# Optimization experiments

Measured on AMD Instinct MI355X. Metric: run time of the kernel, lower is better.

The kernel has to match this reference:

```python
import jax, jax.numpy as jnp
import numpy as np

N_NODES = 100000
N_EDGES = 1600000
IN_DIM = 256
OUT_DIM = 128


def setup_inputs() -> dict:
    key = jax.random.key(0)
    ks = jax.random.split(key, 8)
    x = jax.random.normal(ks[0], (N_NODES, IN_DIM), dtype=jnp.float32)
    # glorot-ish init scaling
    W = jax.random.normal(ks[1], (IN_DIM, OUT_DIM), dtype=jnp.float32) * (6.0 / (IN_DIM + OUT_DIM)) ** 0.5
    fsW = jax.random.normal(ks[2], (IN_DIM, OUT_DIM), dtype=jnp.float32) * (6.0 / (IN_DIM + OUT_DIM)) ** 0.5
    f_weights = jax.random.normal(ks[3], (2 * OUT_DIM, 1), dtype=jnp.float32) * (6.0 / (2 * OUT_DIM + 1)) ** 0.5
    f_bias = jnp.zeros((1,), dtype=jnp.float32)
    # degrees in [1, 64], strictly positive so pow(deg, -p) is finite
    dia_adj = jax.random.uniform(ks[4], (N_NODES,), dtype=jnp.float32) * 63.0 + 1.0
    row = jax.random.randint(ks[5], (N_EDGES,), 0, N_NODES, dtype=jnp.int32)
    col = jax.random.randint(ks[6], (N_EDGES,), 0, N_NODES, dtype=jnp.int32)
    return {"x": x, "W": W, "fsW": fsW, "f_weights": f_weights,
            "f_bias": f_bias, "dia_adj": dia_adj, "row": row, "col": col}


def reference(x, W, fsW, f_weights, f_bias, dia_adj, row, col):
    # pre_sup = x @ weights_, fpre_sup = x @ fs_weights  (dropout=0, dense inputs)
    pre_sup = x @ W                 # [N, out]
    fpre_sup = x @ fsW              # [N, out]
    d = W.shape[1]
    # concat([vi, vj]) @ f_weights == vi @ f_weights[:d] + vj @ f_weights[d:]
    wi, wj = f_weights[:d], f_weights[d:]
    score = jax.nn.sigmoid(fpre_sup[row] @ wi + fpre_sup[col] @ wj + f_bias)  # [E, 1]
    # degree-power normalization: (deg_i * deg_j) ** (-sigmoid_score)
    deg_vivj = (dia_adj[row] * dia_adj[col])[:, None]                         # [E, 1]
    vals = jnp.power(deg_vivj, -score)[:, 0]                                  # [E]
    # sparse matmul: out[r] += vals_e * pre_sup[c] for each edge e=(r,c)
    msg = vals[:, None] * pre_sup[col]                                        # [E, out]
    out = jax.ops.segment_sum(msg, row, num_segments=x.shape[0])              # [N, out]
    return jax.nn.relu(out)
```

## Files before the change

kernel.cpp:

```cpp
#include <hip/hip_runtime.h>

#define N_NODES 100000
#define N_EDGES 1600000
#define IN_DIM 256
#define OUT_DIM 128
#define BROWS 100
#define NBK 1000
#define PBLK 128
#define EPB 12500

typedef __attribute__((ext_vector_type(4))) float f32x4;
typedef __attribute__((ext_vector_type(8))) short s16x8;

__device__ inline unsigned short f2bf(float f) {
    union { float f; unsigned int u; } a; a.f = f;
    unsigned int r = a.u + 0x7fffu + ((a.u >> 16) & 1u);
    return (unsigned short)(r >> 16);
}
__device__ inline float bf2f(unsigned short h) {
    union { unsigned int u; float f; } a; a.u = ((unsigned int)h) << 16;
    return a.f;
}

__global__ __launch_bounds__(256) void kprep(
        const float* __restrict__ fsW, const float* __restrict__ fw,
        const float* __restrict__ W, const int* __restrict__ row,
        float* __restrict__ u, float* __restrict__ v,
        unsigned short* __restrict__ wt, int* __restrict__ hist_t) {
    __shared__ int h[NBK];
    __shared__ float wi[128], wj[128];
    const int t = threadIdx.x, blk = blockIdx.x;
    if (blk < PBLK) {
        wt[blk * 256 + t] = f2bf(W[(size_t)t * 128 + blk]);
        for (int b = t; b < NBK; b += 256) h[b] = 0;
        __syncthreads();
        const int e0 = blk * EPB;
        for (int i = t; i < EPB; i += 256)
            atomicAdd(&h[row[e0 + i] / BROWS], 1);
        __syncthreads();
        for (int b = t; b < NBK; b += 256)
            hist_t[b * PBLK + blk] = h[b];
    } else {
        if (t < 128) wi[t] = fw[t]; else wj[t - 128] = fw[t];
        __syncthreads();
        const float* rowp = fsW + (size_t)t * OUT_DIM;
        float su = 0.f, sv = 0.f;
        for (int d = 0; d < 128; d += 4) {
            float4 a = *(const float4*)(rowp + d);
            su += a.x * wi[d] + a.y * wi[d + 1] + a.z * wi[d + 2] + a.w * wi[d + 3];
            sv += a.x * wj[d] + a.y * wj[d + 1] + a.z * wj[d + 2] + a.w * wj[d + 3];
        }
        u[t] = su; v[t] = sv;
    }
}

__global__ __launch_bounds__(256) void gemm_mfma(
        const float* __restrict__ x, const unsigned short* __restrict__ wt,
        const float* __restrict__ u, const float* __restrict__ v,
        unsigned short* __restrict__ psb, float* __restrict__ si, float* __restrict__ sj) {
    __shared__ unsigned short xa[64 * 136];

    const int t = threadIdx.x;
    const int wave = t >> 6, lane = t & 63;
    const int l15 = lane & 15, lhi = lane >> 4;
    const int row = t >> 2, quad = t & 3;
    const int brow = blockIdx.x * 64;
    const int gnode = brow + row;
    const bool fullblk = (brow + 64 <= N_NODES);
    const bool valid = gnode < N_NODES;

    f32x4 acc[4][2];
#pragma unroll
    for (int mi = 0; mi < 4; ++mi)
#pragma unroll
        for (int ni = 0; ni < 2; ++ni) acc[mi][ni] = (f32x4){0.f, 0.f, 0.f, 0.f};
    float su = 0.f, sv = 0.f;

#pragma unroll
    for (int ph = 0; ph < 2; ++ph) {
        const float* xp = x + (size_t)gnode * IN_DIM + ph * 128 + quad * 32;
        const float* up = u + ph * 128 + quad * 32;
        const float* vp = v + ph * 128 + quad * 32;
        if (fullblk) {
#pragma unroll
            for (int cc = 0; cc < 4; ++cc) {
                float4 a0 = ((const float4*)xp)[cc * 2];
                float4 a1 = ((const float4*)xp)[cc * 2 + 1];
                float4 u0 = ((const float4*)up)[cc * 2], u1 = ((const float4*)up)[cc * 2 + 1];
                float4 v0 = ((const float4*)vp)[cc * 2], v1 = ((const float4*)vp)[cc * 2 + 1];
                su = fmaf(a0.x, u0.x, su); su = fmaf(a0.y, u0.y, su);
                su = fmaf(a0.z, u0.z, su); su = fmaf(a0.w, u0.w, su);
                su = fmaf(a1.x, u1.x, su); su = fmaf(a1.y, u1.y, su);
                su = fmaf(a1.z, u1.z, su); su = fmaf(a1.w, u1.w, su);
                sv = fmaf(a0.x, v0.x, sv); sv = fmaf(a0.y, v0.y, sv);
                sv = fmaf(a0.z, v0.z, sv); sv = fmaf(a0.w, v0.w, sv);
                sv = fmaf(a1.x, v1.x, sv); sv = fmaf(a1.y, v1.y, sv);
                sv = fmaf(a1.z, v1.z, sv); sv = fmaf(a1.w, v1.w, sv);
                union { unsigned short h[8]; uint4 q; } pk;
                pk.h[0] = f2bf(a0.x); pk.h[1] = f2bf(a0.y); pk.h[2] = f2bf(a0.z); pk.h[3] = f2bf(a0.w);
                pk.h[4] = f2bf(a1.x); pk.h[5] = f2bf(a1.y); pk.h[6] = f2bf(a1.z); pk.h[7] = f2bf(a1.w);
                *(uint4*)&xa[row * 136 + quad * 32 + cc * 8] = pk.q;
            }
        } else {
#pragma unroll
            for (int cc = 0; cc < 4; ++cc) {
                float4 a0 = make_float4(0.f, 0.f, 0.f, 0.f), a1 = a0;
                if (valid) {
                    a0 = ((const float4*)xp)[cc * 2];
                    a1 = ((const float4*)xp)[cc * 2 + 1];
                    float4 u0 = ((const float4*)up)[cc * 2], u1 = ((const float4*)up)[cc * 2 + 1];
                    float4 v0 = ((const float4*)vp)[cc * 2], v1 = ((const float4*)vp)[cc * 2 + 1];
                    su = fmaf(a0.x, u0.x, su); su = fmaf(a0.y, u0.y, su);
                    su = fmaf(a0.z, u0.z, su); su = fmaf(a0.w, u0.w, su);
                    su = fmaf(a1.x, u1.x, su); su = fmaf(a1.y, u1.y, su);
                    su = fmaf(a1.z, u1.z, su); su = fmaf(a1.w, u1.w, su);
                    sv = fmaf(a0.x, v0.x, sv); sv = fmaf(a0.y, v0.y, sv);
                    sv = fmaf(a0.z, v0.z, sv); sv = fmaf(a0.w, v0.w, sv);
                    sv = fmaf(a1.x, v1.x, sv); sv = fmaf(a1.y, v1.y, sv);
                    sv = fmaf(a1.z, v1.z, sv); sv = fmaf(a1.w, v1.w, sv);
                }
                union { unsigned short h[8]; uint4 q; } pk;
                pk.h[0] = f2bf(a0.x); pk.h[1] = f2bf(a0.y); pk.h[2] = f2bf(a0.z); pk.h[3] = f2bf(a0.w);
                pk.h[4] = f2bf(a1.x); pk.h[5] = f2bf(a1.y); pk.h[6] = f2bf(a1.z); pk.h[7] = f2bf(a1.w);
                *(uint4*)&xa[row * 136 + quad * 32 + cc * 8] = pk.q;
            }
        }
        __syncthreads();

        {
            const unsigned short* wb0 = wt + (size_t)(wave * 32 + l15) * IN_DIM + ph * 128 + lhi * 8;
            s16x8 bfr[4][2];
#pragma unroll
            for (int ks = 0; ks < 4; ++ks) {
                bfr[ks][0] = *(const s16x8*)(wb0 + ks * 32);
                bfr[ks][1] = *(const s16x8*)(wb0 + (size_t)16 * IN_DIM + ks * 32);
            }
#pragma unroll
            for (int ks = 0; ks < 4; ++ks) {
                const int k0 = ks * 32 + lhi * 8;
                s16x8 afr[4];
#pragma unroll
                for (int mi = 0; mi < 4; ++mi)
                    afr[mi] = *(const s16x8*)&xa[(mi * 16 + l15) * 136 + k0];
#pragma unroll
                for (int mi = 0; mi < 4; ++mi)
#pragma unroll
                    for (int ni = 0; ni < 2; ++ni)
                        acc[mi][ni] = __builtin_amdgcn_mfma_f32_16x16x32_bf16(
                            afr[mi], bfr[ks][ni], acc[mi][ni], 0, 0, 0);
            }
        }
        __syncthreads();
    }

    su += __shfl_xor(su, 1); su += __shfl_xor(su, 2);
    sv += __shfl_xor(sv, 1); sv += __shfl_xor(sv, 2);
    if (quad == 0 && valid) { si[gnode] = su; sj[gnode] = sv; }

    unsigned short* cl = xa;
#pragma unroll
    for (int mi = 0; mi < 4; ++mi)
#pragma unroll
        for (int ni = 0; ni < 2; ++ni) {
            const int colb = wave * 32 + ni * 16 + l15;
#pragma unroll
            for (int j = 0; j < 4; ++j)
                cl[(mi * 16 + lhi * 4 + j) * 128 + colb] = f2bf(acc[mi][ni][j]);
        }
    __syncthreads();
    {
        const int rl = t >> 2;
        const int cb = (t & 3) * 32;
        if (brow + rl < N_NODES) {
            const uint4* src = (const uint4*)&cl[rl * 128 + cb];
            uint4* dst = (uint4*)&psb[(size_t)(brow + rl) * OUT_DIM + cb];
            dst[0] = src[0]; dst[1] = src[1]; dst[2] = src[2]; dst[3] = src[3];
        }
    }
}

__global__ __launch_bounds__(1024) void kbscan(const int* __restrict__ hist_t,
                                               int* __restrict__ bpre) {
    __shared__ int s[1024];
    const int t = threadIdx.x;
    int v = 0;
    if (t < NBK) {
        const int* hp = hist_t + t * PBLK;
        for (int k = 0; k < PBLK; ++k) v += hp[k];
    }
    s[t] = v;
    __syncthreads();
    for (int off = 1; off < 1024; off <<= 1) {
        int nv = (t >= off) ? s[t - off] : 0;
        __syncthreads();
        s[t] += nv;
        __syncthreads();
    }
    if (t < NBK) bpre[t] = s[t] - v;
    if (t == 1023) bpre[NBK] = s[1023];
}

__global__ __launch_bounds__(128) void koff(const int* __restrict__ hist_t,
                                            const int* __restrict__ bpre,
                                            int* __restrict__ off) {
    const int b = blockIdx.x, t = threadIdx.x;
    const int lane = t & 63, w = t >> 6;
    int v = hist_t[b * PBLK + t];
    int s = v;
#pragma unroll
    for (int o = 1; o < 64; o <<= 1) { int tt = __shfl_up(s, o); if (lane >= o) s += tt; }
    __shared__ int ws2[2];
    if (lane == 63) ws2[w] = s;
    __syncthreads();
    int base = (w == 1) ? ws2[0] : 0;
    off[b * PBLK + t] = bpre[b] + base + (s - v);
}

__global__ __launch_bounds__(256) void kpart1(const int* __restrict__ row,
                                              const int* __restrict__ col,
                                              const int* __restrict__ off,
                                              unsigned int* __restrict__ part) {
    __shared__ int cur[NBK];
    const int t = threadIdx.x, blk = blockIdx.x;
    for (int b = t; b < NBK; b += 256) cur[b] = off[b * PBLK + blk];
    __syncthreads();
    const int e0 = blk * EPB;
    for (int i = t; i < EPB; i += 256) {
        int r = row[e0 + i], c = col[e0 + i];
        int b = r / BROWS;
        int rl = r - b * BROWS;
        int pos = atomicAdd(&cur[b], 1);
        part[pos] = ((unsigned)rl << 17) | (unsigned)c;
    }
}

__global__ __launch_bounds__(256) void kpart2(const unsigned int* __restrict__ part,
                                              const int* __restrict__ bpre,
                                              const float* __restrict__ si,
                                              const float* __restrict__ sj,
                                              const float* __restrict__ dia,
                                              const float* __restrict__ fb,
                                              int2* __restrict__ epack,
                                              int* __restrict__ offs,
                                              int* __restrict__ deg) {
    __shared__ int cnt[BROWS];
    __shared__ int cur[BROWS];
    __shared__ float sil[BROWS], dial[BROWS];
    __shared__ int wtot[4];
    const int b = blockIdx.x, t = threadIdx.x;
    const int rbase = b * BROWS;
    if (t < BROWS) {
        cnt[t] = 0;
        sil[t] = si[rbase + t];
        dial[t] = dia[rbase + t];
    }
    __syncthreads();
    const int bstart = bpre[b], bend = bpre[b + 1];
    for (int e = bstart + t; e < bend; e += 256)
        atomicAdd(&cnt[part[e] >> 17], 1);
    __syncthreads();
    {
        int vv = (t < BROWS) ? cnt[t] : 0;
        int lane = t & 63, w = t >> 6;
        int s = vv;
#pragma unroll
        for (int o = 1; o < 64; o <<= 1) { int tt = __shfl_up(s, o); if (lane >= o) s += tt; }
        if (lane == 63) wtot[w] = s;
        __syncthreads();
        int base = 0;
        for (int k = 0; k < w; ++k) base += wtot[k];
        int excl = base + s - vv;
        if (t < BROWS) {
            cur[t] = bstart + excl;
            offs[rbase + t] = bstart + excl;
            deg[rbase + t] = vv;
        }
    }
    __syncthreads();
    const float fbv = fb[0];
    for (int e = bstart + t; e < bend; e += 256) {
        unsigned pk = part[e];
        int rl = (int)(pk >> 17);
        int c = (int)(pk & 0x1FFFFu);
        float tval = sil[rl] + sj[c] + fbv;
        float sg = 1.f / (1.f + expf(-tval));
        float l2 = log2f(dial[rl] * dia[c]);
        float val = exp2f(-sg * l2);
        int pos = atomicAdd(&cur[rl], 1);
        epack[pos] = make_int2(c, __float_as_int(val));
    }
}

__global__ __launch_bounds__(256) void kgather(
        const int* __restrict__ offs, const int* __restrict__ deg,
        const int2* __restrict__ epack,
        const unsigned short* __restrict__ psb, float* __restrict__ out) {
    int lane = threadIdx.x & 31;
    int node = blockIdx.x * 8 + (threadIdx.x >> 5);
    if (node >= N_NODES) return;
    int start = offs[node], d = deg[node];
    const int2* ep = epack + start;
    float a0 = 0.f, a1 = 0.f, a2 = 0.f, a3 = 0.f;
    int k = 0;
    for (; k + 4 <= d; k += 4) {
        int2 e0 = ep[k], e1 = ep[k + 1], e2 = ep[k + 2], e3 = ep[k + 3];
        ushort4 p0 = *(const ushort4*)&psb[(size_t)e0.x * OUT_DIM + lane * 4];
        ushort4 p1 = *(const ushort4*)&psb[(size_t)e1.x * OUT_DIM + lane * 4];
        ushort4 p2 = *(const ushort4*)&psb[(size_t)e2.x * OUT_DIM + lane * 4];
        ushort4 p3 = *(const ushort4*)&psb[(size_t)e3.x * OUT_DIM + lane * 4];
        float v0 = __int_as_float(e0.y), v1 = __int_as_float(e1.y);
        float v2 = __int_as_float(e2.y), v3 = __int_as_float(e3.y);
        a0 = fmaf(v0, bf2f(p0.x), a0); a1 = fmaf(v0, bf2f(p0.y), a1);
        a2 = fmaf(v0, bf2f(p0.z), a2); a3 = fmaf(v0, bf2f(p0.w), a3);
        a0 = fmaf(v1, bf2f(p1.x), a0); a1 = fmaf(v1, bf2f(p1.y), a1);
        a2 = fmaf(v1, bf2f(p1.z), a2); a3 = fmaf(v1, bf2f(p1.w), a3);
        a0 = fmaf(v2, bf2f(p2.x), a0); a1 = fmaf(v2, bf2f(p2.y), a1);
        a2 = fmaf(v2, bf2f(p2.z), a2); a3 = fmaf(v2, bf2f(p2.w), a3);
        a0 = fmaf(v3, bf2f(p3.x), a0); a1 = fmaf(v3, bf2f(p3.y), a1);
        a2 = fmaf(v3, bf2f(p3.z), a2); a3 = fmaf(v3, bf2f(p3.w), a3);
    }
    for (; k < d; ++k) {
        int2 e0 = ep[k];
        float v0 = __int_as_float(e0.y);
        ushort4 p0 = *(const ushort4*)&psb[(size_t)e0.x * OUT_DIM + lane * 4];
        a0 = fmaf(v0, bf2f(p0.x), a0);
        a1 = fmaf(v0, bf2f(p0.y), a1);
        a2 = fmaf(v0, bf2f(p0.z), a2);
        a3 = fmaf(v0, bf2f(p0.w), a3);
    }
    float4 o;
    o.x = fmaxf(a0, 0.f); o.y = fmaxf(a1, 0.f);
    o.z = fmaxf(a2, 0.f); o.w = fmaxf(a3, 0.f);
    *(float4*)&out[(size_t)node * OUT_DIM + lane * 4] = o;
}

extern "C" void kernel_launch(void* const* d_in, const int* in_sizes, int n_in,
                              void* d_out, int out_size, void* d_ws, size_t ws_size,
                              hipStream_t stream) {
    const float* x   = (const float*)d_in[0];
    const float* W   = (const float*)d_in[1];
    const float* fsW = (const float*)d_in[2];
    const float* fw  = (const float*)d_in[3];
    const float* fb  = (const float*)d_in[4];
    const float* dia = (const float*)d_in[5];
    const int*   row = (const int*)d_in[6];
    const int*   col = (const int*)d_in[7];
    float* out = (float*)d_out;

    char* p = (char*)d_ws;
    auto alloc = [&](size_t bytes) -> char* {
        char* r = p; p += (bytes + 255) & ~(size_t)255; return r;
    };
    float* u      = (float*)alloc(256 * 4);
    float* v      = (float*)alloc(256 * 4);
    unsigned short* wtb = (unsigned short*)alloc((size_t)128 * 256 * 2);
    float* si     = (float*)alloc((size_t)N_NODES * 4);
    float* sj     = (float*)alloc((size_t)N_NODES * 4);
    int*   deg    = (int*)alloc((size_t)N_NODES * 4);
    int*   offs   = (int*)alloc((size_t)N_NODES * 4);
    unsigned short* psb = (unsigned short*)alloc((size_t)N_NODES * OUT_DIM * 2);
    int*   hist_t = (int*)alloc((size_t)NBK * PBLK * 4);
    int*   bpre   = (int*)alloc((size_t)(NBK + 1) * 4);
    int*   off    = (int*)alloc((size_t)NBK * PBLK * 4);
    unsigned int* part = (unsigned int*)alloc((size_t)N_EDGES * 4);
    int2*  epack  = (int2*)alloc((size_t)N_EDGES * 8);

    kprep<<<PBLK + 1, 256, 0, stream>>>(fsW, fw, W, row, u, v, wtb, hist_t);
    gemm_mfma<<<(N_NODES + 63) / 64, 256, 0, stream>>>(x, wtb, u, v, psb, si, sj);
    kbscan<<<1, 1024, 0, stream>>>(hist_t, bpre);
    koff<<<NBK, PBLK, 0, stream>>>(hist_t, bpre, off);
    kpart1<<<PBLK, 256, 0, stream>>>(row, col, off, part);
    kpart2<<<NBK, 256, 0, stream>>>(part, bpre, si, sj, dia, fb, epack, offs, deg);
    kgather<<<N_NODES / 8, 256, 0, stream>>>(offs, deg, epack, psb, out);
}
```

Before: 207.2 us.

## Split fp32-to-bf16 conversion from GEMM and load bf16 tiles via global_load_lds

Splits the fused convert+GEMM kernel in two. The first kernel converts x to a padded bf16 buffer and computes the score dot products. The second loads whole 64x256 bf16 tiles straight into LDS with global_load_lds, using an XOR swizzle against bank conflicts, and runs the MFMA loop without a mid-loop barrier. It also vectorizes the histogram-scan sum and unrolls the gather loop to 8 edges. The cost is an extra round trip of the bf16 x buffer through global memory (about 51 MB written and read) plus one more launch. The padded rows of that buffer are never written, so the GEMM reads uninitialised memory for those tail rows.

```diff
diff --git a/kernel.cpp b/kernel.cpp
--- a/kernel.cpp
+++ b/kernel.cpp
@@ -1,6 +1,7 @@
 #include <hip/hip_runtime.h>
 
 #define N_NODES 100000
+#define N_PAD 100032
 #define N_EDGES 1600000
 #define IN_DIM 256
 #define OUT_DIM 128
@@ -20,6 +21,11 @@
 __device__ inline float bf2f(unsigned short h) {
     union { unsigned int u; float f; } a; a.u = ((unsigned int)h) << 16;
     return a.f;
+}
+__device__ inline void gload16(const void* g, void* l) {
+    __builtin_amdgcn_global_load_lds(
+        (const __attribute__((address_space(1))) void*)g,
+        (__attribute__((address_space(3))) void*)l, 16, 0, 0);
 }
 
 __global__ __launch_bounds__(256) void kprep(
@@ -54,108 +60,101 @@
     }
 }
 
-__global__ __launch_bounds__(256) void gemm_mfma(
-        const float* __restrict__ x, const unsigned short* __restrict__ wt,
-        const float* __restrict__ u, const float* __restrict__ v,
-        unsigned short* __restrict__ psb, float* __restrict__ si, float* __restrict__ sj) {
-    __shared__ unsigned short xa[64 * 136];
+__global__ __launch_bounds__(256) void kconv(
+        const float* __restrict__ x, const float* __restrict__ u,
+        const float* __restrict__ v, unsigned short* __restrict__ xb,
+        float* __restrict__ si, float* __restrict__ sj) {
+    const int t = threadIdx.x;
+    const int row = t >> 2, quad = t & 3;
+    const int gnode = blockIdx.x * 64 + row;
+    if (gnode >= N_NODES) return;
+    const float* xp = x + (size_t)gnode * IN_DIM + quad * 64;
+    const float* up = u + quad * 64;
+    const float* vp = v + quad * 64;
+    unsigned short* op = xb + (size_t)gnode * IN_DIM + quad * 64;
+    float su = 0.f, sv = 0.f;
+#pragma unroll
+    for (int c = 0; c < 8; ++c) {
+        float4 a0 = ((const float4*)xp)[c * 2];
+        float4 a1 = ((const float4*)xp)[c * 2 + 1];
+        float4 u0 = ((const float4*)up)[c * 2], u1 = ((const float4*)up)[c * 2 + 1];
+        float4 v0 = ((const float4*)vp)[c * 2], v1 = ((const float4*)vp)[c * 2 + 1];
+        su = fmaf(a0.x, u0.x, su); su = fmaf(a0.y, u0.y, su);
+        su = fmaf(a0.z, u0.z, su); su = fmaf(a0.w, u0.w, su);
+        su = fmaf(a1.x, u1.x, su); su = fmaf(a1.y, u1.y, su);
+        su = fmaf(a1.z, u1.z, su); su = fmaf(a1.w, u1.w, su);
+        sv = fmaf(a0.x, v0.x, sv); sv = fmaf(a0.y, v0.y, sv);
+        sv = fmaf(a0.z, v0.z, sv); sv = fmaf(a0.w, v0.w, sv);
+        sv = fmaf(a1.x, v1.x, sv); sv = fmaf(a1.y, v1.y, sv);
+        sv = fmaf(a1.z, v1.z, sv); sv = fmaf(a1.w, v1.w, sv);
+        union { unsigned short h[8]; uint4 q; } pk;
+        pk.h[0] = f2bf(a0.x); pk.h[1] = f2bf(a0.y); pk.h[2] = f2bf(a0.z); pk.h[3] = f2bf(a0.w);
+        pk.h[4] = f2bf(a1.x); pk.h[5] = f2bf(a1.y); pk.h[6] = f2bf(a1.z); pk.h[7] = f2bf(a1.w);
+        *(uint4*)(op + c * 8) = pk.q;
+    }
+    su += __shfl_xor(su, 1); su += __shfl_xor(su, 2);
+    sv += __shfl_xor(sv, 1); sv += __shfl_xor(sv, 2);
+    if (quad == 0) { si[gnode] = su; sj[gnode] = sv; }
+}
+
+__global__ __launch_bounds__(256) void gemm2(
+        const unsigned short* __restrict__ xb, const unsigned short* __restrict__ wt,
+        unsigned short* __restrict__ psb) {
+    __shared__ unsigned short xa[64 * 256];
 
     const int t = threadIdx.x;
     const int wave = t >> 6, lane = t & 63;
     const int l15 = lane & 15, lhi = lane >> 4;
-    const int row = t >> 2, quad = t & 3;
     const int brow = blockIdx.x * 64;
-    const int gnode = brow + row;
-    const bool fullblk = (brow + 64 <= N_NODES);
-    const bool valid = gnode < N_NODES;
+
+    {
+        const char* src = (const char*)(xb + (size_t)brow * IN_DIM);
+        char* dst = (char*)xa;
+#pragma unroll
+        for (int i = 0; i < 8; ++i) {
+            int lo = i * 4096 + t * 16;
+            int so = lo ^ (((lo >> 9) & 7) << 4);
+            gload16(src + so, dst + lo);
+        }
+    }
 
     f32x4 acc[4][2];
 #pragma unroll
     for (int mi = 0; mi < 4; ++mi)
 #pragma unroll
         for (int ni = 0; ni < 2; ++ni) acc[mi][ni] = (f32x4){0.f, 0.f, 0.f, 0.f};
-    float su = 0.f, sv = 0.f;
-
-#pragma unroll
-    for (int ph = 0; ph < 2; ++ph) {
-        const float* xp = x + (size_t)gnode * IN_DIM + ph * 128 + quad * 32;
-        const float* up = u + ph * 128 + quad * 32;
-        const float* vp = v + ph * 128 + quad * 32;
-        if (fullblk) {
-#pragma unroll
-            for (int cc = 0; cc < 4; ++cc) {
-                float4 a0 = ((const float4*)xp)[cc * 2];
-                float4 a1 = ((const float4*)xp)[cc * 2 + 1];
-                float4 u0 = ((const float4*)up)[cc * 2], u1 = ((const float4*)up)[cc * 2 + 1];
-                float4 v0 = ((const float4*)vp)[cc * 2], v1 = ((const float4*)vp)[cc * 2 + 1];
-                su = fmaf(a0.x, u0.x, su); su = fmaf(a0.y, u0.y, su);
-                su = fmaf(a0.z, u0.z, su); su = fmaf(a0.w, u0.w, su);
-                su = fmaf(a1.x, u1.x, su); su = fmaf(a1.y, u1.y, su);
-                su = fmaf(a1.z, u1.z, su); su = fmaf(a1.w, u1.w, su);
-                sv = fmaf(a0.x, v0.x, sv); sv = fmaf(a0.y, v0.y, sv);
-                sv = fmaf(a0.z, v0.z, sv); sv = fmaf(a0.w, v0.w, sv);
-                sv = fmaf(a1.x, v1.x, sv); sv = fmaf(a1.y, v1.y, sv);
-                sv = fmaf(a1.z, v1.z, sv); sv = fmaf(a1.w, v1.w, sv);
-                union { unsigned short h[8]; uint4 q; } pk;
-                pk.h[0] = f2bf(a0.x); pk.h[1] = f2bf(a0.y); pk.h[2] = f2bf(a0.z); pk.h[3] = f2bf(a0.w);
-                pk.h[4] = f2bf(a1.x); pk.h[5] = f2bf(a1.y); pk.h[6] = f2bf(a1.z); pk.h[7] = f2bf(a1.w);
-                *(uint4*)&xa[row * 136 + quad * 32 + cc * 8] = pk.q;
+
+    __syncthreads();
+
+#pragma unroll
+    for (int g = 0; g < 2; ++g) {
+        const unsigned short* wb0 = wt + (size_t)(wave * 32 + l15) * IN_DIM + g * 128 + lhi * 8;
+        s16x8 bfr[4][2];
+#pragma unroll
+        for (int ks = 0; ks < 4; ++ks) {
+            bfr[ks][0] = *(const s16x8*)(wb0 + ks * 32);
+            bfr[ks][1] = *(const s16x8*)(wb0 + (size_t)16 * IN_DIM + ks * 32);
+        }
+#pragma unroll
+        for (int ks = 0; ks < 4; ++ks) {
+            const int k0 = g * 128 + ks * 32 + lhi * 8;
+            s16x8 afr[4];
+#pragma unroll
+            for (int mi = 0; mi < 4; ++mi) {
+                const int r = mi * 16 + l15;
+                int byte = r * 512 + k0 * 2;
+                byte ^= ((r & 7) << 4);
+                afr[mi] = *(const s16x8*)((const char*)xa + byte);
             }
-        } else {
-#pragma unroll
-            for (int cc = 0; cc < 4; ++cc) {
-                float4 a0 = make_float4(0.f, 0.f, 0.f, 0.f), a1 = a0;
-                if (valid) {
-                    a0 = ((const float4*)xp)[cc * 2];
-                    a1 = ((const float4*)xp)[cc * 2 + 1];
-                    float4 u0 = ((const float4*)up)[cc * 2], u1 = ((const float4*)up)[cc * 2 + 1];
-                    float4 v0 = ((const float4*)vp)[cc * 2], v1 = ((const float4*)vp)[cc * 2 + 1];
-                    su = fmaf(a0.x, u0.x, su); su = fmaf(a0.y, u0.y, su);
-                    su = fmaf(a0.z, u0.z, su); su = fmaf(a0.w, u0.w, su);
-                    su = fmaf(a1.x, u1.x, su); su = fmaf(a1.y, u1.y, su);
-                    su = fmaf(a1.z, u1.z, su); su = fmaf(a1.w, u1.w, su);
-                    sv = fmaf(a0.x, v0.x, sv); sv = fmaf(a0.y, v0.y, sv);
-                    sv = fmaf(a0.z, v0.z, sv); sv = fmaf(a0.w, v0.w, sv);
-                    sv = fmaf(a1.x, v1.x, sv); sv = fmaf(a1.y, v1.y, sv);
-                    sv = fmaf(a1.z, v1.z, sv); sv = fmaf(a1.w, v1.w, sv);
-                }
-                union { unsigned short h[8]; uint4 q; } pk;
-                pk.h[0] = f2bf(a0.x); pk.h[1] = f2bf(a0.y); pk.h[2] = f2bf(a0.z); pk.h[3] = f2bf(a0.w);
-                pk.h[4] = f2bf(a1.x); pk.h[5] = f2bf(a1.y); pk.h[6] = f2bf(a1.z); pk.h[7] = f2bf(a1.w);
-                *(uint4*)&xa[row * 136 + quad * 32 + cc * 8] = pk.q;
-            }
-        }
-        __syncthreads();
-
-        {
-            const unsigned short* wb0 = wt + (size_t)(wave * 32 + l15) * IN_DIM + ph * 128 + lhi * 8;
-            s16x8 bfr[4][2];
-#pragma unroll
-            for (int ks = 0; ks < 4; ++ks) {
-                bfr[ks][0] = *(const s16x8*)(wb0 + ks * 32);
-                bfr[ks][1] = *(const s16x8*)(wb0 + (size_t)16 * IN_DIM + ks * 32);
-            }
-#pragma unroll
-            for (int ks = 0; ks < 4; ++ks) {
-                const int k0 = ks * 32 + lhi * 8;
-                s16x8 afr[4];
-#pragma unroll
-                for (int mi = 0; mi < 4; ++mi)
-                    afr[mi] = *(const s16x8*)&xa[(mi * 16 + l15) * 136 + k0];
-#pragma unroll
-                for (int mi = 0; mi < 4; ++mi)
-#pragma unroll
-                    for (int ni = 0; ni < 2; ++ni)
-                        acc[mi][ni] = __builtin_amdgcn_mfma_f32_16x16x32_bf16(
-                            afr[mi], bfr[ks][ni], acc[mi][ni], 0, 0, 0);
-            }
-        }
-        __syncthreads();
-    }
-
-    su += __shfl_xor(su, 1); su += __shfl_xor(su, 2);
-    sv += __shfl_xor(sv, 1); sv += __shfl_xor(sv, 2);
-    if (quad == 0 && valid) { si[gnode] = su; sj[gnode] = sv; }
+#pragma unroll
+            for (int mi = 0; mi < 4; ++mi)
+#pragma unroll
+                for (int ni = 0; ni < 2; ++ni)
+                    acc[mi][ni] = __builtin_amdgcn_mfma_f32_16x16x32_bf16(
+                        afr[mi], bfr[ks][ni], acc[mi][ni], 0, 0, 0);
+        }
+    }
+    __syncthreads();
 
     unsigned short* cl = xa;
 #pragma unroll
@@ -185,8 +184,12 @@
     const int t = threadIdx.x;
     int v = 0;
     if (t < NBK) {
-        const int* hp = hist_t + t * PBLK;
-        for (int k = 0; k < PBLK; ++k) v += hp[k];
+        const int4* hp = (const int4*)(hist_t + t * PBLK);
+#pragma unroll 4
+        for (int k = 0; k < PBLK / 4; ++k) {
+            int4 a = hp[k];
+            v += a.x + a.y + a.z + a.w;
+        }
     }
     s[t] = v;
     __syncthreads();
@@ -302,14 +305,21 @@
     const int2* ep = epack + start;
     float a0 = 0.f, a1 = 0.f, a2 = 0.f, a3 = 0.f;
     int k = 0;
-    for (; k + 4 <= d; k += 4) {
-        int2 e0 = ep[k], e1 = ep[k + 1], e2 = ep[k + 2], e3 = ep[k + 3];
+    for (; k + 8 <= d; k += 8) {
+        int2 e0 = ep[k],     e1 = ep[k + 1], e2 = ep[k + 2], e3 = ep[k + 3];
+        int2 e4 = ep[k + 4], e5 = ep[k + 5], e6 = ep[k + 6], e7 = ep[k + 7];
         ushort4 p0 = *(const ushort4*)&psb[(size_t)e0.x * OUT_DIM + lane * 4];
         ushort4 p1 = *(const ushort4*)&psb[(size_t)e1.x * OUT_DIM + lane * 4];
         ushort4 p2 = *(const ushort4*)&psb[(size_t)e2.x * OUT_DIM + lane * 4];
         ushort4 p3 = *(const ushort4*)&psb[(size_t)e3.x * OUT_DIM + lane * 4];
+        ushort4 p4 = *(const ushort4*)&psb[(size_t)e4.x * OUT_DIM + lane * 4];
+        ushort4 p5 = *(const ushort4*)&psb[(size_t)e5.x * OUT_DIM + lane * 4];
+        ushort4 p6 = *(const ushort4*)&psb[(size_t)e6.x * OUT_DIM + lane * 4];
+        ushort4 p7 = *(const ushort4*)&psb[(size_t)e7.x * OUT_DIM + lane * 4];
         float v0 = __int_as_float(e0.y), v1 = __int_as_float(e1.y);
         float v2 = __int_as_float(e2.y), v3 = __int_as_float(e3.y);
+        float v4 = __int_as_float(e4.y), v5 = __int_as_float(e5.y);
+        float v6 = __int_as_float(e6.y), v7 = __int_as_float(e7.y);
         a0 = fmaf(v0, bf2f(p0.x), a0); a1 = fmaf(v0, bf2f(p0.y), a1);
         a2 = fmaf(v0, bf2f(p0.z), a2); a3 = fmaf(v0, bf2f(p0.w), a3);
         a0 = fmaf(v1, bf2f(p1.x), a0); a1 = fmaf(v1, bf2f(p1.y), a1);
@@ -318,6 +328,14 @@
         a2 = fmaf(v2, bf2f(p2.z), a2); a3 = fmaf(v2, bf2f(p2.w), a3);
         a0 = fmaf(v3, bf2f(p3.x), a0); a1 = fmaf(v3, bf2f(p3.y), a1);
         a2 = fmaf(v3, bf2f(p3.z), a2); a3 = fmaf(v3, bf2f(p3.w), a3);
+        a0 = fmaf(v4, bf2f(p4.x), a0); a1 = fmaf(v4, bf2f(p4.y), a1);
+        a2 = fmaf(v4, bf2f(p4.z), a2); a3 = fmaf(v4, bf2f(p4.w), a3);
+        a0 = fmaf(v5, bf2f(p5.x), a0); a1 = fmaf(v5, bf2f(p5.y), a1);
+        a2 = fmaf(v5, bf2f(p5.z), a2); a3 = fmaf(v5, bf2f(p5.w), a3);
+        a0 = fmaf(v6, bf2f(p6.x), a0); a1 = fmaf(v6, bf2f(p6.y), a1);
+        a2 = fmaf(v6, bf2f(p6.z), a2); a3 = fmaf(v6, bf2f(p6.w), a3);
+        a0 = fmaf(v7, bf2f(p7.x), a0); a1 = fmaf(v7, bf2f(p7.y), a1);
+        a2 = fmaf(v7, bf2f(p7.z), a2); a3 = fmaf(v7, bf2f(p7.w), a3);
     }
     for (; k < d; ++k) {
         int2 e0 = ep[k];
@@ -358,6 +376,7 @@
     float* sj     = (float*)alloc((size_t)N_NODES * 4);
     int*   deg    = (int*)alloc((size_t)N_NODES * 4);
     int*   offs   = (int*)alloc((size_t)N_NODES * 4);
+    unsigned short* xb  = (unsigned short*)alloc((size_t)N_PAD * IN_DIM * 2);
     unsigned short* psb = (unsigned short*)alloc((size_t)N_NODES * OUT_DIM * 2);
     int*   hist_t = (int*)alloc((size_t)NBK * PBLK * 4);
     int*   bpre   = (int*)alloc((size_t)(NBK + 1) * 4);
@@ -366,7 +385,8 @@
     int2*  epack  = (int2*)alloc((size_t)N_EDGES * 8);
 
     kprep<<<PBLK + 1, 256, 0, stream>>>(fsW, fw, W, row, u, v, wtb, hist_t);
-    gemm_mfma<<<(N_NODES + 63) / 64, 256, 0, stream>>>(x, wtb, u, v, psb, si, sj);
+    kconv<<<(N_NODES + 63) / 64, 256, 0, stream>>>(x, u, v, xb, si, sj);
+    gemm2<<<N_PAD / 64, 256, 0, stream>>>(xb, wtb, psb);
     kbscan<<<1, 1024, 0, stream>>>(hist_t, bpre);
     koff<<<NBK, PBLK, 0, stream>>>(hist_t, bpre, off);
     kpart1<<<PBLK, 256, 0, stream>>>(row, col, off, part);
```

After: 253.1 us. +22.1%, slower.
